# Kernel tuning notes

Measured on AMD Instinct MI355X. Metric: run time of the kernel, lower is better.

Reference implementation:

```python
import jax, jax.numpy as jnp
import numpy as np

EPS = 1e-5  # torch LayerNorm default eps
B, N, D_IN, E, H, V = 4096, 32, 256, 128, 512, 32

def _ln(x):
    # LayerNorm without affine (elementwise_affine=False), biased variance
    m = jnp.mean(x, axis=-1, keepdims=True)
    v = jnp.mean(jnp.square(x - m), axis=-1, keepdims=True)
    return (x - m) * jax.lax.rsqrt(v + EPS)

def _ln_gru_cell(x, h, i2h_W, i2h_b, h2h_W, h2h_b, hW_W, hW_b, hU_W, hU_b):
    gates = jax.nn.sigmoid(_ln(x @ i2h_W + i2h_b) + _ln(h @ h2h_W + h2h_b))  # [B,2H]
    hs = h.shape[-1]
    z_t = gates[:, :hs]
    r_t = gates[:, hs:]
    h_hat = jnp.tanh(_ln(x @ hW_W + hW_b) + r_t * _ln(h @ hU_W + hU_b))
    return (1.0 - z_t) * h + z_t * h_hat

def setup_inputs() -> dict:
    key = jax.random.key(0)
    ks = jax.random.split(key, 32)
    std0 = 1.0 / np.sqrt(H)
    u = lambda k, shp: jax.random.uniform(k, shp, jnp.float32, -std0, std0)
    in0 = 3 * E  # attn context + msg embedding + feedback embedding
    inp = {
        'sender_messages_embedded': jax.random.normal(ks[0], (B, E), jnp.float32),
        'prev_hidden': jax.random.normal(ks[1], (2, B, H), jnp.float32),
        'candidate_objects': jax.random.normal(ks[2], (B, N, D_IN), jnp.float32),
        'prev_msg_embedding': jax.random.normal(ks[3], (B, E), jnp.float32),
        # linear_objects_in_keys
        'Wk': jax.random.normal(ks[4], (D_IN, E), jnp.float32) * 0.05,
        'bk': jnp.zeros((E,), jnp.float32),
        # LayerNormGRUCell layer 0 (input 3E)
        'i2h_W0': u(ks[5], (in0, 2 * H)), 'i2h_b0': u(ks[6], (2 * H,)),
        'h2h_W0': u(ks[7], (H, 2 * H)), 'h2h_b0': u(ks[8], (2 * H,)),
        'hW_W0': u(ks[9], (in0, H)), 'hW_b0': u(ks[10], (H,)),
        'hU_W0': u(ks[11], (H, H)), 'hU_b0': u(ks[12], (H,)),
        # LayerNormGRUCell layer 1 (input H)
        'i2h_W1': u(ks[13], (H, 2 * H)), 'i2h_b1': u(ks[14], (2 * H,)),
        'h2h_W1': u(ks[15], (H, 2 * H)), 'h2h_b1': u(ks[16], (2 * H,)),
        'hW_W1': u(ks[17], (H, H)), 'hW_b1': u(ks[18], (H,)),
        'hU_W1': u(ks[19], (H, H)), 'hU_b1': u(ks[20], (H,)),
        # hidden_to_feedback_output
        'out_W': jax.random.normal(ks[21], (H, V), jnp.float32) * 0.05,
        'out_b': jnp.zeros((V,), jnp.float32),
    }
    return inp

def reference(sender_messages_embedded, prev_hidden, candidate_objects, prev_msg_embedding,
              Wk, bk,
              i2h_W0, i2h_b0, h2h_W0, h2h_b0, hW_W0, hW_b0, hU_W0, hU_b0,
              i2h_W1, i2h_b1, h2h_W1, h2h_b1, hW_W1, hW_b1, hU_W1, hU_b1,
              out_W, out_b):
    # object attention (dot): query = msg embedding, keys = projected candidates
    keys = candidate_objects @ Wk + bk                              # [B,N,E]
    scores = jnp.einsum('be,bne->bn', sender_messages_embedded, keys)
    weights = jax.nn.softmax(scores, axis=1)                        # [B,N]
    context = jnp.einsum('bn,bne->be', weights, keys)               # [B,E]
    rnn_input = jnp.concatenate([context, sender_messages_embedded, prev_msg_embedding], axis=-1)  # [B,3E]
    h0 = _ln_gru_cell(rnn_input, prev_hidden[0], i2h_W0, i2h_b0, h2h_W0, h2h_b0, hW_W0, hW_b0, hU_W0, hU_b0)
    h1 = _ln_gru_cell(h0, prev_hidden[1], i2h_W1, i2h_b1, h2h_W1, h2h_b1, hW_W1, hW_b1, hU_W1, hU_b1)
    logits = h1 @ out_W + out_b                                     # [B,V]
    logp = jax.nn.log_softmax(logits, axis=-1)
    probs = jnp.exp(logp)
    entropy = -jnp.sum(probs * logp, axis=-1)                       # [B]
    output_token = jnp.argmax(probs, axis=-1)                       # eval-mode argmax
    output_token_logits = jnp.take_along_axis(logp, output_token[:, None], axis=1)[:, 0]
    new_hidden = jnp.stack([h0, h1])                                # [2,B,H]
    return (output_token, entropy, output_token_logits, logits, new_hidden)
```

## Files before the change

### kernel.cpp

```cpp
#include <hip/hip_runtime.h>
#include <hip/hip_bf16.h>
#include <math.h>

#define B_SZ   4096
#define NCAND  32
#define DIN    256
#define E_SZ   128
#define H_SZ   512
#define VOCAB  32
#define LN_EPS 1e-5f

typedef unsigned short u16;
typedef unsigned int   u32;
typedef __attribute__((ext_vector_type(8))) short  short8;
typedef __attribute__((ext_vector_type(4))) float  floatx4;

static __device__ __forceinline__ float sigmoidf_(float x) {
    return 1.0f / (1.0f + expf(-x));
}
static __device__ __forceinline__ u16 f2bf(float x) {
    u32 u = __float_as_uint(x);
    return (u16)((u + 0x7FFFu + ((u >> 16) & 1u)) >> 16);
}
static __device__ __forceinline__ float bfbits2f(u16 h) {
    return __uint_as_float(((u32)h) << 16);
}

typedef const __attribute__((address_space(1))) unsigned int* gas_ptr;
typedef __attribute__((address_space(3)))       unsigned int* las_ptr;
static __device__ __forceinline__ void gload_lds16(const u16* g, u16* l) {
    __builtin_amdgcn_global_load_lds((gas_ptr)(const void*)g, (las_ptr)(void*)l, 16, 0, 0);
}

static __device__ __forceinline__ void split_store8(const float* __restrict__ g,
                                                    u16* __restrict__ sh,
                                                    u16* __restrict__ sl)
{
    float4 a = *(const float4*)g;
    float4 b = *(const float4*)(g + 4);
    float v[8] = {a.x, a.y, a.z, a.w, b.x, b.y, b.z, b.w};
    union { u16 us[8]; uint4 q; } hb, lb;
    #pragma unroll
    for (int j = 0; j < 8; ++j) {
        u16 h = f2bf(v[j]);
        hb.us[j] = h;
        lb.us[j] = f2bf(v[j] - bfbits2f(h));
    }
    *(uint4*)sh = hb.q;
    *(uint4*)sl = lb.q;
}


__global__ __launch_bounds__(256)
void transpose_split_w(const float* __restrict__ W1, const float* __restrict__ W2,
                       int N1, int N2, int K,
                       u16* __restrict__ Wt_hi, u16* __restrict__ Wt_lo)
{
    __shared__ float t[64][68];
    const int n0 = blockIdx.x * 64, k0 = blockIdx.y * 64;
    const int tid = threadIdx.x;
    const int KT = K >> 5;

    {
        const int kl = tid >> 4, nl4 = (tid & 15) * 4;
        const int ng = n0 + nl4;
        const float* src; int col, ld;
        if (ng < N1) { src = W1; col = ng;      ld = N1; }
        else         { src = W2; col = ng - N1; ld = N2; }
        #pragma unroll
        for (int p = 0; p < 4; ++p) {
            float4 v = *(const float4*)(src + (size_t)(k0 + kl + p * 16) * ld + col);
            *(float4*)&t[kl + p * 16][nl4] = v;
        }
    }
    __syncthreads();

    const int nl = tid >> 2, kc = tid & 3;
    union { u16 us[16]; uint4 v[2]; } hb, lb;
    #pragma unroll
    for (int j = 0; j < 16; ++j) {
        float x = t[kc * 16 + j][nl];
        u16 h = f2bf(x);
        float r = x - bfbits2f(h);
        hb.us[j] = h;
        lb.us[j] = f2bf(r);
    }
    const int n  = n0 + nl;
    const int kb = k0 + kc * 16;
    const size_t off = ((size_t)(n >> 7) * KT + (kb >> 5)) * 4096
                     + (size_t)(n & 127) * 32 + (kb & 31);
    *(uint4*)(Wt_hi + off)     = hb.v[0];
    *(uint4*)(Wt_hi + off + 8) = hb.v[1];
    *(uint4*)(Wt_lo + off)     = lb.v[0];
    *(uint4*)(Wt_lo + off + 8) = lb.v[1];
}

__global__ __launch_bounds__(256)
void bias_cat4_kernel(const float* __restrict__ a0, const float* __restrict__ c0, float* __restrict__ o0,
                      const float* __restrict__ a1, const float* __restrict__ c1, float* __restrict__ o1,
                      const float* __restrict__ a2, const float* __restrict__ c2, float* __restrict__ o2,
                      const float* __restrict__ a3, const float* __restrict__ c3, float* __restrict__ o3)
{
    const int t = blockIdx.x * 256 + threadIdx.x;
    const int w = t / 1536;
    const int i = t - w * 1536;
    const float* a; const float* c; float* o;
    if      (w == 0) { a = a0; c = c0; o = o0; }
    else if (w == 1) { a = a1; c = c1; o = o1; }
    else if (w == 2) { a = a2; c = c2; o = o2; }
    else             { a = a3; c = c3; o = o3; }
    o[i] = (i < 1024) ? a[i] : c[i - 1024];
}

__global__ __launch_bounds__(256)
void split_blocked_kernel(const float* __restrict__ src,
                          u16* __restrict__ hi, u16* __restrict__ lo)
{
    const int i = blockIdx.x * 256 + threadIdx.x;
    const int m = i >> 6, kq = (i & 63) << 3;
    const size_t idx = ((size_t)(m >> 7) * 16 + (kq >> 5)) * 4096
                     + (size_t)(m & 127) * 32 + (kq & 31);
    split_store8(src + (size_t)m * 512 + kq, &hi[idx], &lo[idx]);
}

__global__ __launch_bounds__(256)
void mfma_gemm_dual_kernel(const u16* __restrict__ Axh, const u16* __restrict__ Axl,
                           const u16* __restrict__ Wxh, const u16* __restrict__ Wxl,
                           const float* __restrict__ bx, float* __restrict__ Cx, int KTx,
                           const u16* __restrict__ Ahh, const u16* __restrict__ Ahl,
                           const u16* __restrict__ Whh, const u16* __restrict__ Whl,
                           const float* __restrict__ bh, float* __restrict__ Ch, int KTh)
{
    __shared__ __align__(16) u16 sAh[2][4096];
    __shared__ __align__(16) u16 sAl[2][4096];
    __shared__ __align__(16) u16 sWh[2][4096];
    __shared__ __align__(16) u16 sWl[2][4096];

    const int tid  = threadIdx.x;
    const int lane = tid & 63;
    const int wave = tid >> 6;
    const int wm = (wave >> 1) * 64;
    const int wn = (wave & 1) * 64;
    const int r16 = lane & 15;
    const int q8  = (lane >> 4) * 8;

    const int f   = blockIdx.x;
    const int lin = (f & 7) * 96 + (f >> 3);
    const int sel = lin >= 384;
    const int r   = lin - (sel ? 384 : 0);
    const int mt  = r / 12;
    const int nt  = r - mt * 12;
    const int m_base = mt * 128;
    const int n_base = nt * 128;

    const u16* Ah_  = sel ? Ahh : Axh;
    const u16* Al_  = sel ? Ahl : Axl;
    const u16* Wh_  = sel ? Whh : Wxh;
    const u16* Wl_  = sel ? Whl : Wxl;
    const float* bias = sel ? bh : bx;
    float*       C    = sel ? Ch : Cx;
    const int    KT   = sel ? KTh : KTx;

    const size_t abase = (size_t)(m_base >> 7) * KT * 4096;
    const size_t wbase = (size_t)(n_base >> 7) * KT * 4096;
    const int sofs = wave * 1024;
    const int gofs = sofs + (lane << 3);

    floatx4 acc[4][4] = {};

    {
        const size_t ai = abase + gofs;
        const size_t wi = wbase + gofs;
        gload_lds16(Ah_ + ai,       &sAh[0][sofs]);
        gload_lds16(Ah_ + ai + 512, &sAh[0][sofs + 512]);
        gload_lds16(Al_ + ai,       &sAl[0][sofs]);
        gload_lds16(Al_ + ai + 512, &sAl[0][sofs + 512]);
        gload_lds16(Wh_ + wi,       &sWh[0][sofs]);
        gload_lds16(Wh_ + wi + 512, &sWh[0][sofs + 512]);
        gload_lds16(Wl_ + wi,       &sWl[0][sofs]);
        gload_lds16(Wl_ + wi + 512, &sWl[0][sofs + 512]);
    }

    int cur = 0;
    for (int kt = 0; kt < KT; ++kt) {
        __syncthreads();

        const int nxt = cur ^ 1;
        if (kt + 1 < KT) {
            const size_t ai = abase + (size_t)(kt + 1) * 4096 + gofs;
            const size_t wi = wbase + (size_t)(kt + 1) * 4096 + gofs;
            gload_lds16(Ah_ + ai,       &sAh[nxt][sofs]);
            gload_lds16(Ah_ + ai + 512, &sAh[nxt][sofs + 512]);
            gload_lds16(Al_ + ai,       &sAl[nxt][sofs]);
            gload_lds16(Al_ + ai + 512, &sAl[nxt][sofs + 512]);
            gload_lds16(Wh_ + wi,       &sWh[nxt][sofs]);
            gload_lds16(Wh_ + wi + 512, &sWh[nxt][sofs + 512]);
            gload_lds16(Wl_ + wi,       &sWl[nxt][sofs]);
            gload_lds16(Wl_ + wi + 512, &sWl[nxt][sofs + 512]);
        }

        short8 ah[4], al[4], bhf[4], blf[4];
        #pragma unroll
        for (int i = 0; i < 4; ++i) {
            const int ar = (wm + i * 16 + r16) * 32 + q8;
            ah[i] = *(const short8*)&sAh[cur][ar];
            al[i] = *(const short8*)&sAl[cur][ar];
            const int br = (wn + i * 16 + r16) * 32 + q8;
            bhf[i] = *(const short8*)&sWh[cur][br];
            blf[i] = *(const short8*)&sWl[cur][br];
        }
        #pragma unroll
        for (int i = 0; i < 4; ++i)
            #pragma unroll
            for (int j = 0; j < 4; ++j) {
                acc[i][j] = __builtin_amdgcn_mfma_f32_16x16x32_bf16(ah[i], bhf[j], acc[i][j], 0, 0, 0);
                acc[i][j] = __builtin_amdgcn_mfma_f32_16x16x32_bf16(ah[i], blf[j], acc[i][j], 0, 0, 0);
                acc[i][j] = __builtin_amdgcn_mfma_f32_16x16x32_bf16(al[i], bhf[j], acc[i][j], 0, 0, 0);
            }

        cur = nxt;
    }

    const int quad = lane >> 4;
    #pragma unroll
    for (int j = 0; j < 4; ++j) {
        const int n = n_base + wn + j * 16 + r16;
        const float bv = bias[n];
        #pragma unroll
        for (int i = 0; i < 4; ++i) {
            #pragma unroll
            for (int rr = 0; rr < 4; ++rr) {
                const int m = m_base + wm + i * 16 + quad * 4 + rr;
                C[(size_t)m * 1536 + n] = acc[i][j][rr] + bv;
            }
        }
    }
}

__global__ __launch_bounds__(256)
void gemm_bt64_kernel(const float* __restrict__ A, const float* __restrict__ Bt,
                      float* __restrict__ C, int M, int N, int K, int ldc)
{
    __shared__ float As[16][68];
    __shared__ float Bs[16][68];

    const int tid = threadIdx.x;
    const int bm = blockIdx.y * 64;
    const int bn = blockIdx.x * 64;
    const int tx = tid & 15, ty = tid >> 4;
    const int m0 = ty * 4, n0 = tx * 4;
    const int arow = tid >> 2, acol = (tid & 3) * 4;

    float acc[4][4] = {};

    for (int k0 = 0; k0 < K; k0 += 16) {
        float4 a4 = *(const float4*)(A  + (size_t)(bm + arow) * K + (k0 + acol));
        float4 b4 = *(const float4*)(Bt + (size_t)(bn + arow) * K + (k0 + acol));
        As[acol + 0][arow] = a4.x; As[acol + 1][arow] = a4.y;
        As[acol + 2][arow] = a4.z; As[acol + 3][arow] = a4.w;
        Bs[acol + 0][arow] = b4.x; Bs[acol + 1][arow] = b4.y;
        Bs[acol + 2][arow] = b4.z; Bs[acol + 3][arow] = b4.w;
        __syncthreads();
        #pragma unroll
        for (int k = 0; k < 16; ++k) {
            float4 av = *(const float4*)&As[k][m0];
            float4 bv = *(const float4*)&Bs[k][n0];
            float aa[4] = {av.x, av.y, av.z, av.w};
            float bb[4] = {bv.x, bv.y, bv.z, bv.w};
            #pragma unroll
            for (int i = 0; i < 4; ++i)
                #pragma unroll
                for (int j = 0; j < 4; ++j)
                    acc[i][j] = fmaf(aa[i], bb[j], acc[i][j]);
        }
        __syncthreads();
    }

    #pragma unroll
    for (int i = 0; i < 4; ++i)
        *(float4*)(C + (size_t)(bm + m0 + i) * ldc + bn + n0) =
            make_float4(acc[i][0], acc[i][1], acc[i][2], acc[i][3]);
}

__global__ __launch_bounds__(256)
void attn_ctx_kernel(const float* __restrict__ co, const float* __restrict__ q,
                     const float* __restrict__ snd, const float* __restrict__ pmsg,
                     float* __restrict__ cbar,
                     u16* __restrict__ rinh, u16* __restrict__ rinl)
{
    __shared__ float s_co[NCAND][264];
    __shared__ float s_q[DIN];
    __shared__ float s_scores[NCAND];
    __shared__ float s_w[NCAND];

    const int b   = blockIdx.x;
    const int tid = threadIdx.x;

    {
        const float4* cop = (const float4*)(co + (size_t)b * NCAND * DIN);
        #pragma unroll
        for (int i = 0; i < 8; ++i) {
            int idx = tid + i * 256;
            float4 v = cop[idx];
            *(float4*)&s_co[idx >> 6][(idx & 63) * 4] = v;
        }
        if (tid < DIN) s_q[tid] = q[(size_t)b * DIN + tid];
    }
    __syncthreads();

    {
        const int n = tid >> 3, part = tid & 7;
        float sc = 0.f;
        #pragma unroll
        for (int qq = 0; qq < 8; ++qq) {
            const int d = part * 4 + qq * 32;
            float4 cv = *(const float4*)&s_co[n][d];
            float4 qv = *(const float4*)&s_q[d];
            sc += cv.x * qv.x + cv.y * qv.y + cv.z * qv.z + cv.w * qv.w;
        }
        #pragma unroll
        for (int m = 4; m; m >>= 1) sc += __shfl_xor(sc, m);
        if (part == 0) s_scores[n] = sc;
    }
    __syncthreads();

    if (tid < NCAND) {
        float s  = s_scores[tid];
        float mx = s;
        #pragma unroll
        for (int m = 16; m; m >>= 1) mx = fmaxf(mx, __shfl_xor(mx, m));
        float e = expf(s - mx);
        float sum = e;
        #pragma unroll
        for (int m = 16; m; m >>= 1) sum += __shfl_xor(sum, m);
        s_w[tid] = e / sum;
    }
    __syncthreads();

    {
        float cb = 0.f;
        #pragma unroll
        for (int n = 0; n < NCAND; ++n) cb = fmaf(s_w[n], s_co[n][tid], cb);
        cbar[(size_t)b * DIN + tid] = cb;
    }
    {
        const float x = (tid < 128) ? snd[(size_t)b * E_SZ + tid]
                                    : pmsg[(size_t)b * E_SZ + (tid - 128)];
        const int d = 128 + tid;
        const u16 h = f2bf(x);
        const u16 l = f2bf(x - bfbits2f(h));
        const size_t idx = ((size_t)(b >> 7) * 12 + (d >> 5)) * 4096
                         + (size_t)(b & 127) * 32 + (d & 31);
        rinh[idx] = h;
        rinl[idx] = l;
    }
}

__global__ __launch_bounds__(256)
void gemm_ctx_kernel(const float* __restrict__ A, const float* __restrict__ Bm,
                     const float* __restrict__ bias,
                     u16* __restrict__ rinh, u16* __restrict__ rinl,
                     int M, int N, int K)
{
    __shared__ float As[16][132];
    __shared__ float Bs[16][68];

    const int tid = threadIdx.x;
    const int bm = blockIdx.y * 128;
    const int bn = blockIdx.x * 64;
    const int tx = tid & 15, ty = tid >> 4;
    const int m0 = ty * 8, n0 = tx * 4;
    const int arow = tid >> 1, acol = (tid & 1) * 8;
    const int brow = tid >> 4, bcol = (tid & 15) * 4;

    float acc[8][4] = {};

    for (int k0 = 0; k0 < K; k0 += 16) {
        float4 a0 = *(const float4*)(A + (size_t)(bm + arow) * K + (k0 + acol));
        float4 a1 = *(const float4*)(A + (size_t)(bm + arow) * K + (k0 + acol + 4));
        float4 b4 = *(const float4*)(Bm + (size_t)(k0 + brow) * N + (bn + bcol));
        As[acol + 0][arow] = a0.x; As[acol + 1][arow] = a0.y;
        As[acol + 2][arow] = a0.z; As[acol + 3][arow] = a0.w;
        As[acol + 4][arow] = a1.x; As[acol + 5][arow] = a1.y;
        As[acol + 6][arow] = a1.z; As[acol + 7][arow] = a1.w;
        *(float4*)&Bs[brow][bcol] = b4;
        __syncthreads();
        #pragma unroll
        for (int k = 0; k < 16; ++k) {
            float4 av0 = *(const float4*)&As[k][m0];
            float4 av1 = *(const float4*)&As[k][m0 + 4];
            float4 bv  = *(const float4*)&Bs[k][n0];
            float aa[8] = {av0.x, av0.y, av0.z, av0.w, av1.x, av1.y, av1.z, av1.w};
            float bb[4] = {bv.x, bv.y, bv.z, bv.w};
            #pragma unroll
            for (int i = 0; i < 8; ++i)
                #pragma unroll
                for (int j = 0; j < 4; ++j)
                    acc[i][j] = fmaf(aa[i], bb[j], acc[i][j]);
        }
        __syncthreads();
    }

    const float4 bv = *(const float4*)(bias + bn + n0);
    #pragma unroll
    for (int i = 0; i < 8; ++i) {
        float o0 = acc[i][0] + bv.x, o1 = acc[i][1] + bv.y;
        float o2 = acc[i][2] + bv.z, o3 = acc[i][3] + bv.w;
        const int m = bm + m0 + i;
        const int d = bn + n0;
        const u16 h0 = f2bf(o0), h1 = f2bf(o1), h2 = f2bf(o2), h3 = f2bf(o3);
        const u16 l0 = f2bf(o0 - bfbits2f(h0));
        const u16 l1 = f2bf(o1 - bfbits2f(h1));
        const u16 l2 = f2bf(o2 - bfbits2f(h2));
        const u16 l3 = f2bf(o3 - bfbits2f(h3));
        const size_t idx = ((size_t)(m >> 7) * 12 + (d >> 5)) * 4096
                         + (size_t)(m & 127) * 32 + (d & 31);
        uint2 hv, lv;
        hv.x = (u32)h0 | ((u32)h1 << 16); hv.y = (u32)h2 | ((u32)h3 << 16);
        lv.x = (u32)l0 | ((u32)l1 << 16); lv.y = (u32)l2 | ((u32)l3 << 16);
        *(uint2*)&rinh[idx] = hv;
        *(uint2*)&rinl[idx] = lv;
    }
}

__global__ __launch_bounds__(256)
void gru_combine_kernel(const float* __restrict__ gxc, const float* __restrict__ ghc,
                        const float* __restrict__ hprev, float* __restrict__ hout,
                        u16* __restrict__ himg_hi, u16* __restrict__ himg_lo)
{
    const int b    = blockIdx.x;
    const int tid  = threadIdx.x;
    const int lane = tid & 63, wv = tid >> 6;

    __shared__ float s_part[4][8];
    __shared__ float s_gates[1024];

    const float* gxb = gxc + (size_t)b * 1536;
    const float* ghb = ghc + (size_t)b * 1536;

    const float4 gx4 = *(const float4*)(gxb + tid * 4);
    const float4 gh4 = *(const float4*)(ghb + tid * 4);
    const float2 cx2 = *(const float2*)(gxb + 1024 + tid * 2);
    const float2 ch2 = *(const float2*)(ghb + 1024 + tid * 2);

    float v[8];
    v[0] = gx4.x + gx4.y + gx4.z + gx4.w;
    v[1] = gx4.x*gx4.x + gx4.y*gx4.y + gx4.z*gx4.z + gx4.w*gx4.w;
    v[2] = gh4.x + gh4.y + gh4.z + gh4.w;
    v[3] = gh4.x*gh4.x + gh4.y*gh4.y + gh4.z*gh4.z + gh4.w*gh4.w;
    v[4] = cx2.x + cx2.y;
    v[5] = cx2.x*cx2.x + cx2.y*cx2.y;
    v[6] = ch2.x + ch2.y;
    v[7] = ch2.x*ch2.x + ch2.y*ch2.y;

    #pragma unroll
    for (int i = 0; i < 8; ++i)
        #pragma unroll
        for (int m = 32; m; m >>= 1) v[i] += __shfl_xor(v[i], m);

    if (lane == 0) {
        #pragma unroll
        for (int i = 0; i < 8; ++i) s_part[wv][i] = v[i];
    }
    __syncthreads();

    float t[8];
    #pragma unroll
    for (int i = 0; i < 8; ++i)
        t[i] = s_part[0][i] + s_part[1][i] + s_part[2][i] + s_part[3][i];

    const float mgx = t[0] / 1024.f;
    const float rgx = 1.f / sqrtf(t[1] / 1024.f - mgx * mgx + LN_EPS);
    const float mgh = t[2] / 1024.f;
    const float rgh = 1.f / sqrtf(t[3] / 1024.f - mgh * mgh + LN_EPS);
    const float mcx = t[4] / 512.f;
    const float rcx = 1.f / sqrtf(t[5] / 512.f - mcx * mcx + LN_EPS);
    const float mch = t[6] / 512.f;
    const float rch = 1.f / sqrtf(t[7] / 512.f - mch * mch + LN_EPS);

    float4 g;
    g.x = sigmoidf_((gx4.x - mgx) * rgx + (gh4.x - mgh) * rgh);
    g.y = sigmoidf_((gx4.y - mgx) * rgx + (gh4.y - mgh) * rgh);
    g.z = sigmoidf_((gx4.z - mgx) * rgx + (gh4.z - mgh) * rgh);
    g.w = sigmoidf_((gx4.w - mgx) * rgx + (gh4.w - mgh) * rgh);
    *(float4*)&s_gates[tid * 4] = g;
    __syncthreads();

    const float2 hp2 = *(const float2*)(hprev + (size_t)b * 512 + tid * 2);
    const float z0 = s_gates[tid * 2 + 0];
    const float z1 = s_gates[tid * 2 + 1];
    const float r0 = s_gates[512 + tid * 2 + 0];
    const float r1 = s_gates[512 + tid * 2 + 1];

    const float hh0 = tanhf((cx2.x - mcx) * rcx + r0 * ((ch2.x - mch) * rch));
    const float hh1 = tanhf((cx2.y - mcx) * rcx + r1 * ((ch2.y - mch) * rch));
    const float hn0 = (1.f - z0) * hp2.x + z0 * hh0;
    const float hn1 = (1.f - z1) * hp2.y + z1 * hh1;

    *(float2*)(hout + (size_t)b * 512 + tid * 2) = make_float2(hn0, hn1);

    if (himg_hi) {
        const u16 h0b = f2bf(hn0), h1b = f2bf(hn1);
        const u16 l0b = f2bf(hn0 - bfbits2f(h0b));
        const u16 l1b = f2bf(hn1 - bfbits2f(h1b));
        const int k = tid * 2;
        const size_t idx = ((size_t)(b >> 7) * 16 + (k >> 5)) * 4096
                         + (size_t)(b & 127) * 32 + (k & 31);
        *(u32*)&himg_hi[idx] = (u32)h0b | ((u32)h1b << 16);
        *(u32*)&himg_lo[idx] = (u32)l0b | ((u32)l1b << 16);
    }
}

__global__ __launch_bounds__(256)
void out_kernel(const float* __restrict__ h1, const float* __restrict__ W,
                const float* __restrict__ bias, float* __restrict__ out)
{
    __shared__ float s_h[4][512];
    const int wave = threadIdx.x >> 6, lane = threadIdx.x & 63;
    const int b = blockIdx.x * 4 + wave;

    {
        const float4* hp = (const float4*)(h1 + (size_t)b * 512);
        float4* sp = (float4*)&s_h[wave][0];
        sp[lane]      = hp[lane];
        sp[lane + 64] = hp[lane + 64];
    }
    __syncthreads();

    const int v = lane & 31, half = lane >> 5;
    float acc = 0.f;
    {
        const float* wp = W + (size_t)half * 256 * 32 + v;
        const float* hh = &s_h[wave][half * 256];
        for (int k = 0; k < 256; ++k) acc = fmaf(hh[k], wp[(size_t)k * 32], acc);
    }
    acc += __shfl_xor(acc, 32);
    const float logit = acc + bias[v];

    if (half == 0)
        out[(size_t)3 * B_SZ + (size_t)b * VOCAB + v] = logit;

    float mval = logit; int midx = v;
    #pragma unroll
    for (int m = 16; m; m >>= 1) {
        float ov = __shfl_xor(mval, m);
        int   oi = __shfl_xor(midx, m);
        if (ov > mval || (ov == mval && oi < midx)) { mval = ov; midx = oi; }
    }
    float ex = expf(logit - mval);
    float sum = ex;
    #pragma unroll
    for (int m = 16; m; m >>= 1) sum += __shfl_xor(sum, m);
    const float lse  = mval + logf(sum);
    const float logp = logit - lse;
    const float p    = expf(logp);
    float epl = p * logp;
    #pragma unroll
    for (int m = 16; m; m >>= 1) epl += __shfl_xor(epl, m);
    const float entropy = -epl;
    const float tok_logp = __shfl(logp, midx, 32);

    if (lane == 0) {
        out[b]             = (float)midx;
        out[B_SZ + b]      = entropy;
        out[2 * B_SZ + b]  = tok_logp;
    }
}

extern "C" void kernel_launch(void* const* d_in, const int* in_sizes, int n_in,
                              void* d_out, int out_size, void* d_ws, size_t ws_size,
                              hipStream_t stream)
{
    const float* snd    = (const float*)d_in[0];
    const float* ph     = (const float*)d_in[1];
    const float* co     = (const float*)d_in[2];
    const float* pmsg   = (const float*)d_in[3];
    const float* Wk     = (const float*)d_in[4];
    const float* bk     = (const float*)d_in[5];
    const float* i2hW0  = (const float*)d_in[6];
    const float* i2hb0  = (const float*)d_in[7];
    const float* h2hW0  = (const float*)d_in[8];
    const float* h2hb0  = (const float*)d_in[9];
    const float* hWW0   = (const float*)d_in[10];
    const float* hWb0   = (const float*)d_in[11];
    const float* hUW0   = (const float*)d_in[12];
    const float* hUb0   = (const float*)d_in[13];
    const float* i2hW1  = (const float*)d_in[14];
    const float* i2hb1  = (const float*)d_in[15];
    const float* h2hW1  = (const float*)d_in[16];
    const float* h2hb1  = (const float*)d_in[17];
    const float* hWW1   = (const float*)d_in[18];
    const float* hWb1   = (const float*)d_in[19];
    const float* hUW1   = (const float*)d_in[20];
    const float* hUb1   = (const float*)d_in[21];
    const float* outW   = (const float*)d_in[22];
    const float* outb   = (const float*)d_in[23];

    float* out = (float*)d_out;
    float* h0out = out + (size_t)3 * B_SZ + (size_t)B_SZ * VOCAB;
    float* h1out = h0out + (size_t)B_SZ * H_SZ;

    const float* h0prev = ph;
    const float* h1prev = ph + (size_t)B_SZ * H_SZ;

    char* p = (char*)d_ws;
    auto alloc_f = [&](size_t n) { float* r = (float*)p; p += n * 4; return r; };
    auto alloc_h = [&](size_t n) { u16* r = (u16*)p; p += ((n * 2 + 15) & ~15ull); return r; };

    float* qbuf   = alloc_f((size_t)B_SZ * 256);
    float* cbar   = alloc_f((size_t)B_SZ * 256);
    float* gxc    = alloc_f((size_t)B_SZ * 1536);
    float* ghc    = alloc_f((size_t)B_SZ * 1536);
    u16* rin_hi = alloc_h((size_t)B_SZ * 384);
    u16* rin_lo = alloc_h((size_t)B_SZ * 384);
    u16* php_hi = alloc_h((size_t)2 * B_SZ * 512);
    u16* php_lo = alloc_h((size_t)2 * B_SZ * 512);
    u16* h0i_hi = alloc_h((size_t)B_SZ * 512);
    u16* h0i_lo = alloc_h((size_t)B_SZ * 512);
    u16* W0x_hi = alloc_h((size_t)1536 * 384);
    u16* W0x_lo = alloc_h((size_t)1536 * 384);
    u16* W0h_hi = alloc_h((size_t)1536 * 512);
    u16* W0h_lo = alloc_h((size_t)1536 * 512);
    u16* W1x_hi = alloc_h((size_t)1536 * 512);
    u16* W1x_lo = alloc_h((size_t)1536 * 512);
    u16* W1h_hi = alloc_h((size_t)1536 * 512);
    u16* W1h_lo = alloc_h((size_t)1536 * 512);
    float* b0x = alloc_f(1536);
    float* b0h = alloc_f(1536);
    float* b1x = alloc_f(1536);
    float* b1h = alloc_f(1536);

    transpose_split_w<<<dim3(24, 6), 256, 0, stream>>>(i2hW0, hWW0, 1024, 512, 384, W0x_hi, W0x_lo);
    transpose_split_w<<<dim3(24, 8), 256, 0, stream>>>(h2hW0, hUW0, 1024, 512, 512, W0h_hi, W0h_lo);
    transpose_split_w<<<dim3(24, 8), 256, 0, stream>>>(i2hW1, hWW1, 1024, 512, 512, W1x_hi, W1x_lo);
    transpose_split_w<<<dim3(24, 8), 256, 0, stream>>>(h2hW1, hUW1, 1024, 512, 512, W1h_hi, W1h_lo);
    bias_cat4_kernel<<<24, 256, 0, stream>>>(i2hb0, hWb0, b0x, h2hb0, hUb0, b0h,
                                             i2hb1, hWb1, b1x, h2hb1, hUb1, b1h);
    split_blocked_kernel<<<2 * B_SZ * 64 / 256, 256, 0, stream>>>(ph, php_hi, php_lo);

    gemm_bt64_kernel<<<dim3(4, 64), 256, 0, stream>>>(snd, Wk, qbuf, B_SZ, 256, 128, 256);
    attn_ctx_kernel<<<B_SZ, 256, 0, stream>>>(co, qbuf, snd, pmsg, cbar, rin_hi, rin_lo);
    gemm_ctx_kernel<<<dim3(2, 32), 256, 0, stream>>>(cbar, Wk, bk, rin_hi, rin_lo, B_SZ, 128, 256);

    mfma_gemm_dual_kernel<<<768, 256, 0, stream>>>(
        rin_hi, rin_lo, W0x_hi, W0x_lo, b0x, gxc, 12,
        php_hi, php_lo, W0h_hi, W0h_lo, b0h, ghc, 16);
    gru_combine_kernel<<<B_SZ, 256, 0, stream>>>(gxc, ghc, h0prev, h0out, h0i_hi, h0i_lo);

    mfma_gemm_dual_kernel<<<768, 256, 0, stream>>>(
        h0i_hi, h0i_lo, W1x_hi, W1x_lo, b1x, gxc, 16,
        php_hi + (size_t)B_SZ * 512, php_lo + (size_t)B_SZ * 512,
        W1h_hi, W1h_lo, b1h, ghc, 16);
    gru_combine_kernel<<<B_SZ, 256, 0, stream>>>(gxc, ghc, h1prev, h1out, (u16*)nullptr, (u16*)nullptr);

    out_kernel<<<B_SZ / 4, 256, 0, stream>>>(h1out, outW, outb, out);
}
```

Baseline: 453.7 us.

## Fuse query and context projections into the attention kernel

Removes the two separate small GEMM kernels that computed q = Wk·snd per batch row and ctx = cbar·Wk, and instead does both matrix-vector products inside the per-batch attention kernel using shared memory. This eliminates two launches and the qbuf/cbar round trips through global memory. In exchange, each of the 4096 blocks re-reads the full 128 KB Wk matrix (once for q, once for ctx, mostly from cache) with scalar FMA matvecs, which can cost more than the original tiled GEMMs.

```diff
diff --git a/kernel.cpp b/kernel.cpp
--- a/kernel.cpp
+++ b/kernel.cpp
@@ -238,60 +238,18 @@
 }
 
 __global__ __launch_bounds__(256)
-void gemm_bt64_kernel(const float* __restrict__ A, const float* __restrict__ Bt,
-                      float* __restrict__ C, int M, int N, int K, int ldc)
-{
-    __shared__ float As[16][68];
-    __shared__ float Bs[16][68];
-
-    const int tid = threadIdx.x;
-    const int bm = blockIdx.y * 64;
-    const int bn = blockIdx.x * 64;
-    const int tx = tid & 15, ty = tid >> 4;
-    const int m0 = ty * 4, n0 = tx * 4;
-    const int arow = tid >> 2, acol = (tid & 3) * 4;
-
-    float acc[4][4] = {};
-
-    for (int k0 = 0; k0 < K; k0 += 16) {
-        float4 a4 = *(const float4*)(A  + (size_t)(bm + arow) * K + (k0 + acol));
-        float4 b4 = *(const float4*)(Bt + (size_t)(bn + arow) * K + (k0 + acol));
-        As[acol + 0][arow] = a4.x; As[acol + 1][arow] = a4.y;
-        As[acol + 2][arow] = a4.z; As[acol + 3][arow] = a4.w;
-        Bs[acol + 0][arow] = b4.x; Bs[acol + 1][arow] = b4.y;
-        Bs[acol + 2][arow] = b4.z; Bs[acol + 3][arow] = b4.w;
-        __syncthreads();
-        #pragma unroll
-        for (int k = 0; k < 16; ++k) {
-            float4 av = *(const float4*)&As[k][m0];
-            float4 bv = *(const float4*)&Bs[k][n0];
-            float aa[4] = {av.x, av.y, av.z, av.w};
-            float bb[4] = {bv.x, bv.y, bv.z, bv.w};
-            #pragma unroll
-            for (int i = 0; i < 4; ++i)
-                #pragma unroll
-                for (int j = 0; j < 4; ++j)
-                    acc[i][j] = fmaf(aa[i], bb[j], acc[i][j]);
-        }
-        __syncthreads();
-    }
-
-    #pragma unroll
-    for (int i = 0; i < 4; ++i)
-        *(float4*)(C + (size_t)(bm + m0 + i) * ldc + bn + n0) =
-            make_float4(acc[i][0], acc[i][1], acc[i][2], acc[i][3]);
-}
-
-__global__ __launch_bounds__(256)
-void attn_ctx_kernel(const float* __restrict__ co, const float* __restrict__ q,
-                     const float* __restrict__ snd, const float* __restrict__ pmsg,
-                     float* __restrict__ cbar,
+void attn_ctx_kernel(const float* __restrict__ co, const float* __restrict__ snd,
+                     const float* __restrict__ pmsg,
+                     const float* __restrict__ Wk, const float* __restrict__ bk,
                      u16* __restrict__ rinh, u16* __restrict__ rinl)
 {
     __shared__ float s_co[NCAND][264];
+    __shared__ float s_snd[E_SZ];
     __shared__ float s_q[DIN];
     __shared__ float s_scores[NCAND];
     __shared__ float s_w[NCAND];
+    __shared__ float s_cb[DIN];
+    __shared__ float s_ctx[2][E_SZ];
 
     const int b   = blockIdx.x;
     const int tid = threadIdx.x;
@@ -304,7 +262,23 @@
             float4 v = cop[idx];
             *(float4*)&s_co[idx >> 6][(idx & 63) * 4] = v;
         }
-        if (tid < DIN) s_q[tid] = q[(size_t)b * DIN + tid];
+        if (tid < E_SZ) s_snd[tid] = snd[(size_t)b * E_SZ + tid];
+    }
+    __syncthreads();
+
+    {
+        const float* wrow = Wk + (size_t)tid * E_SZ;
+        float a0 = 0.f, a1 = 0.f;
+        #pragma unroll
+        for (int e = 0; e < E_SZ; e += 8) {
+            float4 w0 = *(const float4*)(wrow + e);
+            float4 w1 = *(const float4*)(wrow + e + 4);
+            float4 s0 = *(const float4*)&s_snd[e];
+            float4 s1 = *(const float4*)&s_snd[e + 4];
+            a0 += w0.x*s0.x + w0.y*s0.y + w0.z*s0.z + w0.w*s0.w;
+            a1 += w1.x*s1.x + w1.y*s1.y + w1.z*s1.z + w1.w*s1.w;
+        }
+        s_q[tid] = a0 + a1;
     }
     __syncthreads();
 
@@ -341,85 +315,38 @@
         float cb = 0.f;
         #pragma unroll
         for (int n = 0; n < NCAND; ++n) cb = fmaf(s_w[n], s_co[n][tid], cb);
-        cbar[(size_t)b * DIN + tid] = cb;
-    }
-    {
-        const float x = (tid < 128) ? snd[(size_t)b * E_SZ + tid]
-                                    : pmsg[(size_t)b * E_SZ + (tid - 128)];
-        const int d = 128 + tid;
+        s_cb[tid] = cb;
+    }
+    __syncthreads();
+
+    {
+        const int e = tid & 127, h = tid >> 7;
+        const float* wp  = Wk + (size_t)(h * 128) * E_SZ + e;
+        const float* cbp = &s_cb[h * 128];
+        float a0 = 0.f, a1 = 0.f, a2 = 0.f, a3 = 0.f;
+        for (int d = 0; d < 128; d += 4) {
+            a0 = fmaf(cbp[d + 0], wp[(size_t)(d + 0) * E_SZ], a0);
+            a1 = fmaf(cbp[d + 1], wp[(size_t)(d + 1) * E_SZ], a1);
+            a2 = fmaf(cbp[d + 2], wp[(size_t)(d + 2) * E_SZ], a2);
+            a3 = fmaf(cbp[d + 3], wp[(size_t)(d + 3) * E_SZ], a3);
+        }
+        s_ctx[h][e] = (a0 + a1) + (a2 + a3);
+    }
+    __syncthreads();
+
+    const size_t rowbase = (size_t)(b >> 7) * 12 * 4096 + (size_t)(b & 127) * 32;
+    auto put = [&](int d, float x) {
         const u16 h = f2bf(x);
         const u16 l = f2bf(x - bfbits2f(h));
-        const size_t idx = ((size_t)(b >> 7) * 12 + (d >> 5)) * 4096
-                         + (size_t)(b & 127) * 32 + (d & 31);
+        const size_t idx = rowbase + (size_t)(d >> 5) * 4096 + (d & 31);
         rinh[idx] = h;
         rinl[idx] = l;
-    }
-}
-
-__global__ __launch_bounds__(256)
-void gemm_ctx_kernel(const float* __restrict__ A, const float* __restrict__ Bm,
-                     const float* __restrict__ bias,
-                     u16* __restrict__ rinh, u16* __restrict__ rinl,
-                     int M, int N, int K)
-{
-    __shared__ float As[16][132];
-    __shared__ float Bs[16][68];
-
-    const int tid = threadIdx.x;
-    const int bm = blockIdx.y * 128;
-    const int bn = blockIdx.x * 64;
-    const int tx = tid & 15, ty = tid >> 4;
-    const int m0 = ty * 8, n0 = tx * 4;
-    const int arow = tid >> 1, acol = (tid & 1) * 8;
-    const int brow = tid >> 4, bcol = (tid & 15) * 4;
-
-    float acc[8][4] = {};
-
-    for (int k0 = 0; k0 < K; k0 += 16) {
-        float4 a0 = *(const float4*)(A + (size_t)(bm + arow) * K + (k0 + acol));
-        float4 a1 = *(const float4*)(A + (size_t)(bm + arow) * K + (k0 + acol + 4));
-        float4 b4 = *(const float4*)(Bm + (size_t)(k0 + brow) * N + (bn + bcol));
-        As[acol + 0][arow] = a0.x; As[acol + 1][arow] = a0.y;
-        As[acol + 2][arow] = a0.z; As[acol + 3][arow] = a0.w;
-        As[acol + 4][arow] = a1.x; As[acol + 5][arow] = a1.y;
-        As[acol + 6][arow] = a1.z; As[acol + 7][arow] = a1.w;
-        *(float4*)&Bs[brow][bcol] = b4;
-        __syncthreads();
-        #pragma unroll
-        for (int k = 0; k < 16; ++k) {
-            float4 av0 = *(const float4*)&As[k][m0];
-            float4 av1 = *(const float4*)&As[k][m0 + 4];
-            float4 bv  = *(const float4*)&Bs[k][n0];
-            float aa[8] = {av0.x, av0.y, av0.z, av0.w, av1.x, av1.y, av1.z, av1.w};
-            float bb[4] = {bv.x, bv.y, bv.z, bv.w};
-            #pragma unroll
-            for (int i = 0; i < 8; ++i)
-                #pragma unroll
-                for (int j = 0; j < 4; ++j)
-                    acc[i][j] = fmaf(aa[i], bb[j], acc[i][j]);
-        }
-        __syncthreads();
-    }
-
-    const float4 bv = *(const float4*)(bias + bn + n0);
-    #pragma unroll
-    for (int i = 0; i < 8; ++i) {
-        float o0 = acc[i][0] + bv.x, o1 = acc[i][1] + bv.y;
-        float o2 = acc[i][2] + bv.z, o3 = acc[i][3] + bv.w;
-        const int m = bm + m0 + i;
-        const int d = bn + n0;
-        const u16 h0 = f2bf(o0), h1 = f2bf(o1), h2 = f2bf(o2), h3 = f2bf(o3);
-        const u16 l0 = f2bf(o0 - bfbits2f(h0));
-        const u16 l1 = f2bf(o1 - bfbits2f(h1));
-        const u16 l2 = f2bf(o2 - bfbits2f(h2));
-        const u16 l3 = f2bf(o3 - bfbits2f(h3));
-        const size_t idx = ((size_t)(m >> 7) * 12 + (d >> 5)) * 4096
-                         + (size_t)(m & 127) * 32 + (d & 31);
-        uint2 hv, lv;
-        hv.x = (u32)h0 | ((u32)h1 << 16); hv.y = (u32)h2 | ((u32)h3 << 16);
-        lv.x = (u32)l0 | ((u32)l1 << 16); lv.y = (u32)l2 | ((u32)l3 << 16);
-        *(uint2*)&rinh[idx] = hv;
-        *(uint2*)&rinl[idx] = lv;
+    };
+    if (tid < 128) {
+        put(tid, s_ctx[0][tid] + s_ctx[1][tid] + bk[tid]);
+        put(256 + tid, pmsg[(size_t)b * E_SZ + tid]);
+    } else {
+        put(tid, s_snd[tid - 128]);
     }
 }
 
@@ -607,8 +534,6 @@
     auto alloc_f = [&](size_t n) { float* r = (float*)p; p += n * 4; return r; };
     auto alloc_h = [&](size_t n) { u16* r = (u16*)p; p += ((n * 2 + 15) & ~15ull); return r; };
 
-    float* qbuf   = alloc_f((size_t)B_SZ * 256);
-    float* cbar   = alloc_f((size_t)B_SZ * 256);
     float* gxc    = alloc_f((size_t)B_SZ * 1536);
     float* ghc    = alloc_f((size_t)B_SZ * 1536);
     u16* rin_hi = alloc_h((size_t)B_SZ * 384);
@@ -638,9 +563,7 @@
                                              i2hb1, hWb1, b1x, h2hb1, hUb1, b1h);
     split_blocked_kernel<<<2 * B_SZ * 64 / 256, 256, 0, stream>>>(ph, php_hi, php_lo);
 
-    gemm_bt64_kernel<<<dim3(4, 64), 256, 0, stream>>>(snd, Wk, qbuf, B_SZ, 256, 128, 256);
-    attn_ctx_kernel<<<B_SZ, 256, 0, stream>>>(co, qbuf, snd, pmsg, cbar, rin_hi, rin_lo);
-    gemm_ctx_kernel<<<dim3(2, 32), 256, 0, stream>>>(cbar, Wk, bk, rin_hi, rin_lo, B_SZ, 128, 256);
+    attn_ctx_kernel<<<B_SZ, 256, 0, stream>>>(co, snd, pmsg, Wk, bk, rin_hi, rin_lo);
 
     mfma_gemm_dual_kernel<<<768, 256, 0, stream>>>(
         rin_hi, rin_lo, W0x_hi, W0x_lo, b0x, gxc, 12,
```

Measured after the change: 498.5 us. 9.9% more time.
